# Optimization experiments

Hardware: AMD Instinct MI355X
Metric: run time of the kernel (lower is better)

The kernel has to match this reference:

```python
import jax, jax.numpy as jnp
import numpy as np

# Dimensions: T total prefill tokens, S ragged segments (one adapter each),
# M target modules sharing this linear, r LoRA rank.
T, D_IN, D_OUT, R, M, S = 8192, 4096, 4096, 16, 2, 8


def setup_inputs() -> dict:
    key = jax.random.key(0)
    ks = jax.random.split(key, 6)
    x = jax.random.normal(ks[0], (T, D_IN), dtype=jnp.float32)
    W = jax.random.normal(ks[1], (D_OUT, D_IN), dtype=jnp.float32) * 0.02
    b = jax.random.normal(ks[2], (D_OUT,), dtype=jnp.float32) * 0.02
    # lora_A[m, s] = A.T of adapter s for target module m: [D_IN, R]
    lora_A = jax.random.normal(ks[3], (M, S, D_IN, R), dtype=jnp.float32) * 0.02
    # lora_B[m, s] = B.T: [R, D_OUT]
    lora_B = jax.random.normal(ks[4], (M, S, R, D_OUT), dtype=jnp.float32) * 0.02
    cu = jnp.sort(jax.random.randint(ks[5], (S + 1,), 0, T + 1, dtype=jnp.int32))
    cu = cu.at[0].set(0).at[-1].set(T)  # segment boundaries cover [0, T)
    return {"x": x, "W": W, "b": b, "lora_A": lora_A, "lora_B": lora_B,
            "cu_seqlen": cu}


def reference(x, W, b, lora_A, lora_B, cu_seqlen):
    # Base linear: out = x @ W.T + b
    out = x @ W.T + b
    tok = jnp.arange(x.shape[0])
    n_seg = lora_A.shape[1]
    # SGMV-style ragged LoRA: tokens in segment s use adapter s for every
    # target module m; contributions from all modules add into `out`.
    # Masking (instead of dynamic slicing) keeps shapes static / jit-friendly
    # and is exact: masked-out tokens contribute zero.
    for s in range(n_seg):
        mask = ((tok >= cu_seqlen[s]) & (tok < cu_seqlen[s + 1]))
        xm = x * mask.astype(x.dtype)[:, None]            # [T, D_IN], zero outside segment
        u = jnp.einsum('td,mdr->tmr', xm, lora_A[:, s])    # [T, M, R] low-rank down-proj
        out = out + jnp.einsum('tmr,mrD->tD', u, lora_B[:, s])  # up-proj, sum over modules
    return out
```

## Files before the change

kernel.cpp:

```cpp
#include <hip/hip_runtime.h>
#include <hip/hip_bf16.h>

#define T_TOK 8192
#define DIN   4096
#define DOUT  4096
#define RANK  16
#define NMOD  2
#define NSEG  8

typedef __attribute__((ext_vector_type(8))) short bf16x8;
typedef __attribute__((ext_vector_type(8))) unsigned short u16x8;
typedef __attribute__((ext_vector_type(4))) float f32x4;

__device__ inline unsigned short f2bf(float f) {
    union { float f; unsigned u; } v; v.f = f;
    unsigned r = v.u + 0x7FFFu + ((v.u >> 16) & 1u);
    return (unsigned short)(r >> 16);
}

__device__ inline void gload_lds16(const void* g, void* l) {
    __builtin_amdgcn_global_load_lds(
        (const __attribute__((address_space(1))) void*)g,
        (__attribute__((address_space(3))) void*)l, 16, 0, 0);
}

__global__ void cast2_bf16_kernel(const float* __restrict__ sa,
                                  unsigned short* __restrict__ da, int n8a,
                                  const float* __restrict__ sb,
                                  unsigned short* __restrict__ db, int n8b) {
    int i = blockIdx.x * blockDim.x + threadIdx.x;
    const float* s;
    unsigned short* d;
    size_t j;
    if (i < n8a) { s = sa; d = da; j = (size_t)i; }
    else if (i < n8a + n8b) { s = sb; d = db; j = (size_t)(i - n8a); }
    else return;
    const float4* s4 = (const float4*)s;
    float4 a = s4[2 * j];
    float4 b = s4[2 * j + 1];
    u16x8 o;
    o[0] = f2bf(a.x); o[1] = f2bf(a.y); o[2] = f2bf(a.z); o[3] = f2bf(a.w);
    o[4] = f2bf(b.x); o[5] = f2bf(b.y); o[6] = f2bf(b.z); o[7] = f2bf(b.w);
    *(u16x8*)(d + 8 * j) = o;
}

__global__ void prep_A_kernel(const float* __restrict__ A,
                              unsigned short* __restrict__ At) {
    int idx = blockIdx.x * 256 + threadIdx.x;
    int d   = idx & (DIN - 1);
    int smr = idx >> 12;
    int s   = smr >> 5, mr = smr & 31;
    int m   = mr >> 4,  r  = mr & 15;
    float v = A[(((size_t)(m * NSEG + s) * DIN) + d) * RANK + r];
    At[idx] = f2bf(v);
}

__global__ void prep_B_kernel(const float* __restrict__ B,
                              unsigned short* __restrict__ Bt) {
    int o  = blockIdx.x * 256 + threadIdx.x;
    int s  = o >> 12;
    int oc = o & (DOUT - 1);
    unsigned short tmp[32];
    for (int m = 0; m < NMOD; ++m)
        for (int r = 0; r < RANK; ++r)
            tmp[m * 16 + r] =
                f2bf(B[(((size_t)(m * NSEG + s) * RANK) + r) * DOUT + oc]);
    for (int k = 0; k < 4; ++k) {
        u16x8 v;
        for (int j = 0; j < 8; ++j) v[j] = tmp[k * 8 + j];
        *(u16x8*)(Bt + (size_t)o * 32 + k * 8) = v;
    }
}

__global__ __launch_bounds__(64) void u_gemm_kernel(
    const unsigned short* __restrict__ xb, const unsigned short* __restrict__ At,
    const int* __restrict__ cu, float* __restrict__ Pu) {
    int tile = blockIdx.x;
    int ky   = blockIdx.y;
    int lane = threadIdx.x;
    int l15  = lane & 15, lk = lane >> 4;
    int t0   = tile * 32;
    f32x4 acc[2][2] = {};
    bf16x8 zero = {};
    for (int s = 0; s < NSEG; ++s) {
        int lo = cu[s], hi = cu[s + 1];
        if (hi <= t0 || lo >= t0 + 32) continue;
        const unsigned short* atb = At + (size_t)(s * 32) * DIN;
        for (int kt = 0; kt < 32; ++kt) {
            int k0 = ky * 1024 + kt * 32 + lk * 8;
            bf16x8 a[2], b[2];
            for (int mi = 0; mi < 2; ++mi) {
                int row = t0 + mi * 16 + l15;
                bf16x8 av = *(const bf16x8*)(xb + (size_t)row * DIN + k0);
                a[mi] = (row >= lo && row < hi) ? av : zero;
            }
            for (int ni = 0; ni < 2; ++ni) {
                int mr = ni * 16 + l15;
                b[ni] = *(const bf16x8*)(atb + (size_t)mr * DIN + k0);
            }
            for (int mi = 0; mi < 2; ++mi)
                for (int ni = 0; ni < 2; ++ni)
                    acc[mi][ni] = __builtin_amdgcn_mfma_f32_16x16x32_bf16(
                        a[mi], b[ni], acc[mi][ni], 0, 0, 0);
        }
    }
    for (int mi = 0; mi < 2; ++mi)
        for (int ni = 0; ni < 2; ++ni)
            for (int j = 0; j < 4; ++j) {
                int t  = t0 + mi * 16 + lk * 4 + j;
                int mr = ni * 16 + l15;
                Pu[((size_t)ky * T_TOK + t) * 32 + mr] = acc[mi][ni][j];
            }
}

__global__ void reduce_u_kernel(const float* __restrict__ Pu,
                                unsigned short* __restrict__ ub) {
    int idx = blockIdx.x * 256 + threadIdx.x;
    const size_t STRIDE = (size_t)T_TOK * 32;
    float s = Pu[idx] + Pu[idx + STRIDE] + Pu[idx + 2 * STRIDE] + Pu[idx + 3 * STRIDE];
    ub[idx] = f2bf(s);
}


__device__ __forceinline__ bf16x8 lds_frag(const char* tile, int row, int lk) {
    int rb = (row << 6) + (lk << 4);
    rb ^= ((rb >> 7) & 7) << 4;
    return *(const bf16x8*)(tile + rb);
}

__device__ __forceinline__ void stage_chunk(const unsigned short* gbase,
                                            char* lds_tile, int chunkbase, int tid) {
    int tb = chunkbase + tid * 16;
    int gb = tb ^ (((tb >> 7) & 7) << 4);
    int row = gb >> 6;
    int col = (gb & 63) >> 1;
    gload_lds16(gbase + (size_t)row * DIN + col, lds_tile + tb);
}

#define STAGE(T_)                                                              \
  {                                                                            \
    int k0s_ = (T_) * 32;                                                      \
    char* dst_ = lds + ((T_) & 3) * 32768;                                     \
    stage_chunk(xrow + k0s_, dst_, 0, tid);                                    \
    stage_chunk(xrow + k0s_, dst_, 8192, tid);                                 \
    stage_chunk(wrow_g + k0s_, dst_ + 16384, 0, tid);                          \
    stage_chunk(wrow_g + k0s_, dst_ + 16384, 8192, tid);                       \
  }

#define READ_AF2(T_)                                                           \
  {                                                                            \
    const char* Asl_ = lds + ((T_) & 3) * 32768;                               \
    for (int m = 0; m < 4; ++m)                                                \
        af2[m] = lds_frag(Asl_, wrow + (4 + m) * 16 + l15, lk);                \
  }

#define READ_MAIN(BFR_, AF_, T_)                                               \
  {                                                                            \
    const char* Asl_ = lds + ((T_) & 3) * 32768;                               \
    const char* Bsl_ = Asl_ + 16384;                                           \
    for (int n = 0; n < 4; ++n)                                                \
        BFR_[n] = lds_frag(Bsl_, wcol + n * 16 + l15, lk);                     \
    for (int m = 0; m < 4; ++m)                                                \
        AF_[m] = lds_frag(Asl_, wrow + m * 16 + l15, lk);                      \
  }

#define CLUSTER(BFR_, AF_)                                                     \
  {                                                                            \
    __builtin_amdgcn_s_setprio(1);                                             \
    for (int m = 0; m < 4; ++m)                                                \
        for (int n = 0; n < 4; ++n)                                            \
            acc[m][n] = __builtin_amdgcn_mfma_f32_16x16x32_bf16(               \
                AF_[m], BFR_[n], acc[m][n], 0, 0, 0);                          \
    for (int m = 0; m < 4; ++m)                                                \
        for (int n = 0; n < 4; ++n)                                            \
            acc[4 + m][n] = __builtin_amdgcn_mfma_f32_16x16x32_bf16(           \
                af2[m], BFR_[n], acc[4 + m][n], 0, 0, 0);                      \
    __builtin_amdgcn_s_setprio(0);                                             \
  }

#define ITER(UB_, UA_, RB_, RA_, T_, STG_, VM_)                                \
  {                                                                            \
    READ_AF2(T_);                                                              \
    READ_MAIN(RB_, RA_, (T_) + 1);                                             \
    if (STG_) STAGE((T_) + 3);                                                 \
    __builtin_amdgcn_sched_barrier(0);                                         \
    CLUSTER(UB_, UA_);                                                         \
    if ((VM_) == 4)      asm volatile("s_waitcnt vmcnt(4)" ::: "memory");      \
    else if ((VM_) == 0) asm volatile("s_waitcnt vmcnt(0)" ::: "memory");      \
    if ((VM_) >= 0) __builtin_amdgcn_s_barrier();                              \
  }

__global__ __launch_bounds__(512, 2) void main_gemm_kernel(
    const unsigned short* __restrict__ xb, const unsigned short* __restrict__ wb,
    const unsigned short* __restrict__ ub, const unsigned short* __restrict__ bt,
    const float* __restrict__ bias, const int* __restrict__ cu,
    float* __restrict__ out) {
    __shared__ __attribute__((aligned(1024))) char lds[131072];
    int tid  = threadIdx.x;
    int w    = tid >> 6, lane = tid & 63;
    int l15  = lane & 15, lk = lane >> 4;
    int wrow = (w >> 2) * 128;
    int wcol = (w & 3) * 64;
    int swz  = (blockIdx.x & 7) * 64 + (blockIdx.x >> 3);
    int row0 = (swz >> 4) * 256;
    int col0 = (swz & 15) * 256;

    const unsigned short* xrow   = xb + (size_t)row0 * DIN;
    const unsigned short* wrow_g = wb + (size_t)col0 * DIN;

    f32x4 acc[8][4] = {};
    bf16x8 bfrA[4], afA[4], bfrB[4], afB[4], af2[4];

    STAGE(0); STAGE(1); STAGE(2);
    asm volatile("s_waitcnt vmcnt(4)" ::: "memory");
    __builtin_amdgcn_s_barrier();
    READ_MAIN(bfrA, afA, 0);

    #pragma unroll 1
    for (int t = 0; t < 124; t += 2) {
        ITER(bfrA, afA, bfrB, afB, t,     1, 4);
        ITER(bfrB, afB, bfrA, afA, t + 1, 1, 4);
    }
    ITER(bfrA, afA, bfrB, afB, 124, 1, 4);
    ITER(bfrB, afB, bfrA, afA, 125, 0, 0);
    ITER(bfrA, afA, bfrB, afB, 126, 0, -1);
    { READ_AF2(127); __builtin_amdgcn_sched_barrier(0); CLUSTER(bfrB, afB); }

    bf16x8 zero = {};
    for (int s = 0; s < NSEG; ++s) {
        int lo = cu[s], hi = cu[s + 1];
        if (hi <= row0 || lo >= row0 + 256) continue;
        bf16x8 au[8], bu[4];
        for (int m = 0; m < 8; ++m) {
            int row = row0 + wrow + m * 16 + l15;
            bf16x8 v = *(const bf16x8*)(ub + (size_t)row * 32 + lk * 8);
            au[m] = (row >= lo && row < hi) ? v : zero;
        }
        for (int n = 0; n < 4; ++n) {
            int col = col0 + wcol + n * 16 + l15;
            bu[n] = *(const bf16x8*)(bt + ((size_t)s * DOUT + col) * 32 + lk * 8);
        }
        for (int m = 0; m < 8; ++m)
            for (int n = 0; n < 4; ++n)
                acc[m][n] = __builtin_amdgcn_mfma_f32_16x16x32_bf16(
                    au[m], bu[n], acc[m][n], 0, 0, 0);
    }

    float bv[4];
    for (int n = 0; n < 4; ++n) bv[n] = bias[col0 + wcol + n * 16 + l15];
    for (int m = 0; m < 8; ++m) {
        int rbase = row0 + wrow + m * 16 + lk * 4;
        for (int n = 0; n < 4; ++n) {
            int col = col0 + wcol + n * 16 + l15;
            for (int jj = 0; jj < 4; ++jj)
                out[(size_t)(rbase + jj) * DOUT + col] = acc[m][n][jj] + bv[n];
        }
    }
}

extern "C" void kernel_launch(void* const* d_in, const int* in_sizes, int n_in,
                              void* d_out, int out_size, void* d_ws, size_t ws_size,
                              hipStream_t stream) {
    const float* x  = (const float*)d_in[0];
    const float* W  = (const float*)d_in[1];
    const float* b  = (const float*)d_in[2];
    const float* lA = (const float*)d_in[3];
    const float* lB = (const float*)d_in[4];
    const int*   cu = (const int*)d_in[5];
    float* out = (float*)d_out;

    char* ws = (char*)d_ws;
    unsigned short* xb = (unsigned short*)(ws);
    unsigned short* wb = (unsigned short*)(ws + 67108864);
    unsigned short* At = (unsigned short*)(ws + 100663296);
    unsigned short* Bt = (unsigned short*)(ws + 102760448);
    float*          Pu = (float*)(ws + 104857600);
    unsigned short* ub = (unsigned short*)(ws + 109051904);

    const int n8x = T_TOK * DIN / 8, n8w = DOUT * DIN / 8;
    cast2_bf16_kernel<<<(n8x + n8w) / 256, 256, 0, stream>>>(x, xb, n8x, W, wb, n8w);
    prep_A_kernel<<<(NSEG * 32 * DIN) / 256, 256, 0, stream>>>(lA, At);
    prep_B_kernel<<<(NSEG * DOUT) / 256, 256, 0, stream>>>(lB, Bt);
    dim3 ug(T_TOK / 32, 4);
    u_gemm_kernel<<<ug, 64, 0, stream>>>(xb, At, cu, Pu);
    reduce_u_kernel<<<(T_TOK * 32) / 256, 256, 0, stream>>>(Pu, ub);
    dim3 mg(32 * 16);
    main_gemm_kernel<<<mg, 512, 0, stream>>>(xb, wb, ub, Bt, b, cu, out);
}
```

Measured before the change: 326.6 us.

## Switch main GEMM from 16x16x32 to 32x32x16 bf16 MFMA tiles

Replaces the 16x16x32 MFMA tiling of the per-wave 128x64 output tile with 32x32x16 instructions, restructuring the LDS fragment reads, accumulator layout, LoRA up-projection MFMAs and the epilogue store mapping. The larger MFMA shape needs fewer LDS fragment loads per FLOP and fewer instructions, aiming to raise matrix-core throughput. The cost is a different register layout for the accumulators and a more scattered epilogue write pattern, and the 32-wide instructions have longer latency to hide.

```diff
diff --git a/kernel.cpp b/kernel.cpp
--- a/kernel.cpp
+++ b/kernel.cpp
@@ -11,6 +11,7 @@
 typedef __attribute__((ext_vector_type(8))) short bf16x8;
 typedef __attribute__((ext_vector_type(8))) unsigned short u16x8;
 typedef __attribute__((ext_vector_type(4))) float f32x4;
+typedef __attribute__((ext_vector_type(16))) float f32x16;
 
 __device__ inline unsigned short f2bf(float f) {
     union { float f; unsigned u; } v; v.f = f;
@@ -122,8 +123,8 @@
 }
 
 
-__device__ __forceinline__ bf16x8 lds_frag(const char* tile, int row, int lk) {
-    int rb = (row << 6) + (lk << 4);
+__device__ __forceinline__ bf16x8 lds_frag32(const char* tile, int row, int kb) {
+    int rb = (row << 6) + kb;
     rb ^= ((rb >> 7) & 7) << 4;
     return *(const bf16x8*)(tile + rb);
 }
@@ -147,41 +148,43 @@
     stage_chunk(wrow_g + k0s_, dst_ + 16384, 8192, tid);                       \
   }
 
-#define READ_AF2(T_)                                                           \
+#define READ_AH1(T_)                                                           \
   {                                                                            \
     const char* Asl_ = lds + ((T_) & 3) * 32768;                               \
     for (int m = 0; m < 4; ++m)                                                \
-        af2[m] = lds_frag(Asl_, wrow + (4 + m) * 16 + l15, lk);                \
-  }
-
-#define READ_MAIN(BFR_, AF_, T_)                                               \
+        af2[m] = lds_frag32(Asl_, wrow + m * 32 + l31, 32 + kb16);             \
+  }
+
+#define READ_NEXT(BFR_, AF_, T_)                                               \
   {                                                                            \
     const char* Asl_ = lds + ((T_) & 3) * 32768;                               \
     const char* Bsl_ = Asl_ + 16384;                                           \
-    for (int n = 0; n < 4; ++n)                                                \
-        BFR_[n] = lds_frag(Bsl_, wcol + n * 16 + l15, lk);                     \
+    for (int n = 0; n < 2; ++n) {                                              \
+        BFR_[n][0] = lds_frag32(Bsl_, wcol + n * 32 + l31, kb16);              \
+        BFR_[n][1] = lds_frag32(Bsl_, wcol + n * 32 + l31, 32 + kb16);         \
+    }                                                                          \
     for (int m = 0; m < 4; ++m)                                                \
-        AF_[m] = lds_frag(Asl_, wrow + m * 16 + l15, lk);                      \
+        AF_[m] = lds_frag32(Asl_, wrow + m * 32 + l31, kb16);                  \
   }
 
 #define CLUSTER(BFR_, AF_)                                                     \
   {                                                                            \
     __builtin_amdgcn_s_setprio(1);                                             \
     for (int m = 0; m < 4; ++m)                                                \
-        for (int n = 0; n < 4; ++n)                                            \
-            acc[m][n] = __builtin_amdgcn_mfma_f32_16x16x32_bf16(               \
-                AF_[m], BFR_[n], acc[m][n], 0, 0, 0);                          \
+        for (int n = 0; n < 2; ++n)                                            \
+            acc[m][n] = __builtin_amdgcn_mfma_f32_32x32x16_bf16(               \
+                AF_[m], BFR_[n][0], acc[m][n], 0, 0, 0);                       \
     for (int m = 0; m < 4; ++m)                                                \
-        for (int n = 0; n < 4; ++n)                                            \
-            acc[4 + m][n] = __builtin_amdgcn_mfma_f32_16x16x32_bf16(           \
-                af2[m], BFR_[n], acc[4 + m][n], 0, 0, 0);                      \
+        for (int n = 0; n < 2; ++n)                                            \
+            acc[m][n] = __builtin_amdgcn_mfma_f32_32x32x16_bf16(               \
+                af2[m], BFR_[n][1], acc[m][n], 0, 0, 0);                       \
     __builtin_amdgcn_s_setprio(0);                                             \
   }
 
 #define ITER(UB_, UA_, RB_, RA_, T_, STG_, VM_)                                \
   {                                                                            \
-    READ_AF2(T_);                                                              \
-    READ_MAIN(RB_, RA_, (T_) + 1);                                             \
+    READ_AH1(T_);                                                              \
+    READ_NEXT(RB_, RA_, (T_) + 1);                                             \
     if (STG_) STAGE((T_) + 3);                                                 \
     __builtin_amdgcn_sched_barrier(0);                                         \
     CLUSTER(UB_, UA_);                                                         \
@@ -198,7 +201,8 @@
     __shared__ __attribute__((aligned(1024))) char lds[131072];
     int tid  = threadIdx.x;
     int w    = tid >> 6, lane = tid & 63;
-    int l15  = lane & 15, lk = lane >> 4;
+    int l31  = lane & 31;
+    int kb16 = (lane >> 5) * 16;
     int wrow = (w >> 2) * 128;
     int wcol = (w & 3) * 64;
     int swz  = (blockIdx.x & 7) * 64 + (blockIdx.x >> 3);
@@ -208,13 +212,13 @@
     const unsigned short* xrow   = xb + (size_t)row0 * DIN;
     const unsigned short* wrow_g = wb + (size_t)col0 * DIN;
 
-    f32x4 acc[8][4] = {};
-    bf16x8 bfrA[4], afA[4], bfrB[4], afB[4], af2[4];
+    f32x16 acc[4][2] = {};
+    bf16x8 bfrA[2][2], afA[4], bfrB[2][2], afB[4], af2[4];
 
     STAGE(0); STAGE(1); STAGE(2);
     asm volatile("s_waitcnt vmcnt(4)" ::: "memory");
     __builtin_amdgcn_s_barrier();
-    READ_MAIN(bfrA, afA, 0);
+    READ_NEXT(bfrA, afA, 0);
 
     #pragma unroll 1
     for (int t = 0; t < 124; t += 2) {
@@ -224,36 +228,47 @@
     ITER(bfrA, afA, bfrB, afB, 124, 1, 4);
     ITER(bfrB, afB, bfrA, afA, 125, 0, 0);
     ITER(bfrA, afA, bfrB, afB, 126, 0, -1);
-    { READ_AF2(127); __builtin_amdgcn_sched_barrier(0); CLUSTER(bfrB, afB); }
+    { READ_AH1(127); __builtin_amdgcn_sched_barrier(0); CLUSTER(bfrB, afB); }
 
     bf16x8 zero = {};
     for (int s = 0; s < NSEG; ++s) {
         int lo = cu[s], hi = cu[s + 1];
         if (hi <= row0 || lo >= row0 + 256) continue;
-        bf16x8 au[8], bu[4];
-        for (int m = 0; m < 8; ++m) {
-            int row = row0 + wrow + m * 16 + l15;
-            bf16x8 v = *(const bf16x8*)(ub + (size_t)row * 32 + lk * 8);
-            au[m] = (row >= lo && row < hi) ? v : zero;
+        bf16x8 au[4][2], bu[2][2];
+        for (int m = 0; m < 4; ++m) {
+            int row = row0 + wrow + m * 32 + l31;
+            const char* ubase = (const char*)ub + (size_t)row * 64;
+            bf16x8 v0 = *(const bf16x8*)(ubase + kb16);
+            bf16x8 v1 = *(const bf16x8*)(ubase + 32 + kb16);
+            bool in = (row >= lo && row < hi);
+            au[m][0] = in ? v0 : zero;
+            au[m][1] = in ? v1 : zero;
         }
-        for (int n = 0; n < 4; ++n) {
-            int col = col0 + wcol + n * 16 + l15;
-            bu[n] = *(const bf16x8*)(bt + ((size_t)s * DOUT + col) * 32 + lk * 8);
+        for (int n = 0; n < 2; ++n) {
+            int col = col0 + wcol + n * 32 + l31;
+            const char* bbase = (const char*)bt + ((size_t)s * DOUT + col) * 64;
+            bu[n][0] = *(const bf16x8*)(bbase + kb16);
+            bu[n][1] = *(const bf16x8*)(bbase + 32 + kb16);
         }
-        for (int m = 0; m < 8; ++m)
-            for (int n = 0; n < 4; ++n)
-                acc[m][n] = __builtin_amdgcn_mfma_f32_16x16x32_bf16(
-                    au[m], bu[n], acc[m][n], 0, 0, 0);
-    }
-
-    float bv[4];
-    for (int n = 0; n < 4; ++n) bv[n] = bias[col0 + wcol + n * 16 + l15];
-    for (int m = 0; m < 8; ++m) {
-        int rbase = row0 + wrow + m * 16 + lk * 4;
-        for (int n = 0; n < 4; ++n) {
-            int col = col0 + wcol + n * 16 + l15;
-            for (int jj = 0; jj < 4; ++jj)
-                out[(size_t)(rbase + jj) * DOUT + col] = acc[m][n][jj] + bv[n];
+        for (int h = 0; h < 2; ++h)
+            for (int m = 0; m < 4; ++m)
+                for (int n = 0; n < 2; ++n)
+                    acc[m][n] = __builtin_amdgcn_mfma_f32_32x32x16_bf16(
+                        au[m][h], bu[n][h], acc[m][n], 0, 0, 0);
+    }
+
+    float bv[2];
+    for (int n = 0; n < 2; ++n) bv[n] = bias[col0 + wcol + n * 32 + l31];
+    int rsub = 4 * (lane >> 5);
+    for (int m = 0; m < 4; ++m) {
+        int rbase = row0 + wrow + m * 32 + rsub;
+        for (int n = 0; n < 2; ++n) {
+            int col = col0 + wcol + n * 32 + l31;
+            #pragma unroll
+            for (int r = 0; r < 16; ++r) {
+                int row = rbase + (r & 3) + 8 * (r >> 2);
+                out[(size_t)row * DOUT + col] = acc[m][n][r] + bv[n];
+            }
         }
     }
 }
```

Result: slower. 353.5 us (+8.2%).

## Restructure main GEMM into 64-wide K double-buffer with four-phase ping-pong schedule

Applied to the files above, without the earlier changes.

The main bf16 GEMM loop moves from a 4-deep ring of 32-wide K tiles to a 2-deep double buffer of 64-wide K tiles. Each K step is split into four MFMA phases, each with a barrier and a priority bump. Global-to-LDS staging for the next tile is interleaved across those phases, and the LDS swizzle uses 128-byte rows. The aim is fewer loop iterations and better overlap of loads with MFMA work, at the cost of more barriers per step and a shallower prefetch depth.

```diff
diff --git a/kernel.cpp b/kernel.cpp
--- a/kernel.cpp
+++ b/kernel.cpp
@@ -122,72 +122,87 @@
 }
 
 
-__device__ __forceinline__ bf16x8 lds_frag(const char* tile, int row, int lk) {
-    int rb = (row << 6) + (lk << 4);
+__device__ __forceinline__ bf16x8 frag(const char* mat, int row, int kbyte) {
+    int rb = (row << 7) + kbyte;
     rb ^= ((rb >> 7) & 7) << 4;
-    return *(const bf16x8*)(tile + rb);
-}
-
-__device__ __forceinline__ void stage_chunk(const unsigned short* gbase,
-                                            char* lds_tile, int chunkbase, int tid) {
-    int tb = chunkbase + tid * 16;
-    int gb = tb ^ (((tb >> 7) & 7) << 4);
-    int row = gb >> 6;
-    int col = (gb & 63) >> 1;
-    gload_lds16(gbase + (size_t)row * DIN + col, lds_tile + tb);
-}
-
-#define STAGE(T_)                                                              \
+    return *(const bf16x8*)(mat + rb);
+}
+
+#define STAGE_B(SB_, C_, K0_)                                                  \
+  { int tb = tid * 16;                                                         \
+    int lrow = (C_)*64 + (tb >> 7);                                            \
+    int cb = (tb & 127) ^ ((lrow & 7) << 4);                                   \
+    gload_lds16(wrow_g + (size_t)lrow * DIN + (K0_) + (cb >> 1),               \
+                (SB_) + (C_)*8192 + tb); }
+
+#define STAGE_A(SA_, C_, GB_, K0_)                                             \
+  { int tb = tid * 16;                                                         \
+    int lrow = (C_)*64 + (tb >> 7);                                            \
+    int cb = (tb & 127) ^ ((lrow & 7) << 4);                                   \
+    gload_lds16(xrow + (size_t)((GB_) + (tb >> 7)) * DIN + (K0_) + (cb >> 1),  \
+                (SA_) + (C_)*8192 + tb); }
+
+#define VMC(N_)                                                                \
+    if ((N_) == 2)      asm volatile("s_waitcnt vmcnt(2)" ::: "memory");       \
+    else if ((N_) == 0) asm volatile("s_waitcnt vmcnt(0)" ::: "memory");
+
+#define PH_TAIL(VM_)                                                           \
+    __builtin_amdgcn_s_barrier();                                              \
+    asm volatile("s_waitcnt lgkmcnt(0)" ::: "memory");                         \
+    __builtin_amdgcn_sched_barrier(0);                                         \
+    __builtin_amdgcn_s_setprio(1);
+
+#define PH_END(VM_)                                                            \
+    __builtin_amdgcn_s_setprio(0);                                             \
+    VMC(VM_);                                                                  \
+    __builtin_amdgcn_s_barrier();
+
+#define KSTEP(T_, CB_, STG_, VM0_, VM3_)                                       \
   {                                                                            \
-    int k0s_ = (T_) * 32;                                                      \
-    char* dst_ = lds + ((T_) & 3) * 32768;                                     \
-    stage_chunk(xrow + k0s_, dst_, 0, tid);                                    \
-    stage_chunk(xrow + k0s_, dst_, 8192, tid);                                 \
-    stage_chunk(wrow_g + k0s_, dst_ + 16384, 0, tid);                          \
-    stage_chunk(wrow_g + k0s_, dst_ + 16384, 8192, tid);                       \
-  }
-
-#define READ_AF2(T_)                                                           \
-  {                                                                            \
-    const char* Asl_ = lds + ((T_) & 3) * 32768;                               \
+    const char* cA  = lds + (CB_)*65536;                                       \
+    const char* cBm = cA + 32768;                                              \
+    char* sA = lds + (1 - (CB_))*65536;                                        \
+    char* sB = sA + 32768;                                                     \
+    const int k0n = ((T_) + 1) * 64;                                           \
+    bf16x8 af[4], bf0[4], bf1[4];                                              \
+    \
+    for (int n = 0; n < 4; ++n) bf0[n] = frag(cBm, wcol + n*16 + l15, lk*16);  \
+    for (int m = 0; m < 4; ++m) af[m]  = frag(cA, whalf*64 + m*16 + l15, lk*16);\
+    if (STG_) { STAGE_B(sB, 0, k0n); STAGE_B(sB, 1, k0n); }                    \
+    PH_TAIL(VM0_);                                                             \
+    for (int m = 0; m < 4; ++m) for (int n = 0; n < 4; ++n)                    \
+        acc[m][n] = __builtin_amdgcn_mfma_f32_16x16x32_bf16(                   \
+            af[m], bf0[n], acc[m][n], 0, 0, 0);                                \
+    PH_END(VM0_);                                                              \
+           \
     for (int m = 0; m < 4; ++m)                                                \
-        af2[m] = lds_frag(Asl_, wrow + (4 + m) * 16 + l15, lk);                \
-  }
-
-#define READ_MAIN(BFR_, AF_, T_)                                               \
-  {                                                                            \
-    const char* Asl_ = lds + ((T_) & 3) * 32768;                               \
-    const char* Bsl_ = Asl_ + 16384;                                           \
+        af[m] = frag(cA, 128 + whalf*64 + m*16 + l15, lk*16);                  \
+    if (STG_) { STAGE_B(sB, 2, k0n); STAGE_B(sB, 3, k0n); }                    \
+    PH_TAIL(-1);                                                               \
+    for (int m = 0; m < 4; ++m) for (int n = 0; n < 4; ++n)                    \
+        acc[4 + m][n] = __builtin_amdgcn_mfma_f32_16x16x32_bf16(               \
+            af[m], bf0[n], acc[4 + m][n], 0, 0, 0);                            \
+    PH_END(-1);                                                                \
+    \
     for (int n = 0; n < 4; ++n)                                                \
-        BFR_[n] = lds_frag(Bsl_, wcol + n * 16 + l15, lk);                     \
+        bf1[n] = frag(cBm, wcol + n*16 + l15, 64 + lk*16);                     \
     for (int m = 0; m < 4; ++m)                                                \
-        AF_[m] = lds_frag(Asl_, wrow + m * 16 + l15, lk);                      \
-  }
-
-#define CLUSTER(BFR_, AF_)                                                     \
-  {                                                                            \
-    __builtin_amdgcn_s_setprio(1);                                             \
+        af[m] = frag(cA, whalf*64 + m*16 + l15, 64 + lk*16);                   \
+    if (STG_) { STAGE_A(sA, 0, 0, k0n); STAGE_A(sA, 1, 128, k0n); }            \
+    PH_TAIL(-1);                                                               \
+    for (int m = 0; m < 4; ++m) for (int n = 0; n < 4; ++n)                    \
+        acc[m][n] = __builtin_amdgcn_mfma_f32_16x16x32_bf16(                   \
+            af[m], bf1[n], acc[m][n], 0, 0, 0);                                \
+    PH_END(-1);                                                                \
+           \
     for (int m = 0; m < 4; ++m)                                                \
-        for (int n = 0; n < 4; ++n)                                            \
-            acc[m][n] = __builtin_amdgcn_mfma_f32_16x16x32_bf16(               \
-                AF_[m], BFR_[n], acc[m][n], 0, 0, 0);                          \
-    for (int m = 0; m < 4; ++m)                                                \
-        for (int n = 0; n < 4; ++n)                                            \
-            acc[4 + m][n] = __builtin_amdgcn_mfma_f32_16x16x32_bf16(           \
-                af2[m], BFR_[n], acc[4 + m][n], 0, 0, 0);                      \
-    __builtin_amdgcn_s_setprio(0);                                             \
-  }
-
-#define ITER(UB_, UA_, RB_, RA_, T_, STG_, VM_)                                \
-  {                                                                            \
-    READ_AF2(T_);                                                              \
-    READ_MAIN(RB_, RA_, (T_) + 1);                                             \
-    if (STG_) STAGE((T_) + 3);                                                 \
-    __builtin_amdgcn_sched_barrier(0);                                         \
-    CLUSTER(UB_, UA_);                                                         \
-    if ((VM_) == 4)      asm volatile("s_waitcnt vmcnt(4)" ::: "memory");      \
-    else if ((VM_) == 0) asm volatile("s_waitcnt vmcnt(0)" ::: "memory");      \
-    if ((VM_) >= 0) __builtin_amdgcn_s_barrier();                              \
+        af[m] = frag(cA, 128 + whalf*64 + m*16 + l15, 64 + lk*16);             \
+    if (STG_) { STAGE_A(sA, 2, 64, k0n); STAGE_A(sA, 3, 192, k0n); }           \
+    PH_TAIL(VM3_);                                                             \
+    for (int m = 0; m < 4; ++m) for (int n = 0; n < 4; ++n)                    \
+        acc[4 + m][n] = __builtin_amdgcn_mfma_f32_16x16x32_bf16(               \
+            af[m], bf1[n], acc[4 + m][n], 0, 0, 0);                            \
+    PH_END(VM3_);                                                              \
   }
 
 __global__ __launch_bounds__(512, 2) void main_gemm_kernel(
@@ -196,11 +211,12 @@
     const float* __restrict__ bias, const int* __restrict__ cu,
     float* __restrict__ out) {
     __shared__ __attribute__((aligned(1024))) char lds[131072];
-    int tid  = threadIdx.x;
-    int w    = tid >> 6, lane = tid & 63;
-    int l15  = lane & 15, lk = lane >> 4;
-    int wrow = (w >> 2) * 128;
-    int wcol = (w & 3) * 64;
+    int tid   = threadIdx.x;
+    int w     = tid >> 6, lane = tid & 63;
+    int l15   = lane & 15, lk = lane >> 4;
+    int whalf = w >> 2;
+    int wrow  = whalf * 128;
+    int wcol  = (w & 3) * 64;
     int swz  = (blockIdx.x & 7) * 64 + (blockIdx.x >> 3);
     int row0 = (swz >> 4) * 256;
     int col0 = (swz & 15) * 256;
@@ -209,22 +225,25 @@
     const unsigned short* wrow_g = wb + (size_t)col0 * DIN;
 
     f32x4 acc[8][4] = {};
-    bf16x8 bfrA[4], afA[4], bfrB[4], afB[4], af2[4];
-
-    STAGE(0); STAGE(1); STAGE(2);
-    asm volatile("s_waitcnt vmcnt(4)" ::: "memory");
+
+    {
+        char* sA = lds;
+        char* sB = lds + 32768;
+        STAGE_B(sB, 0, 0); STAGE_B(sB, 1, 0);
+        STAGE_B(sB, 2, 0); STAGE_B(sB, 3, 0);
+        STAGE_A(sA, 0, 0, 0); STAGE_A(sA, 1, 128, 0);
+        STAGE_A(sA, 2, 64, 0); STAGE_A(sA, 3, 192, 0);
+    }
+    asm volatile("s_waitcnt vmcnt(2)" ::: "memory");
     __builtin_amdgcn_s_barrier();
-    READ_MAIN(bfrA, afA, 0);
 
     #pragma unroll 1
-    for (int t = 0; t < 124; t += 2) {
-        ITER(bfrA, afA, bfrB, afB, t,     1, 4);
-        ITER(bfrB, afB, bfrA, afA, t + 1, 1, 4);
-    }
-    ITER(bfrA, afA, bfrB, afB, 124, 1, 4);
-    ITER(bfrB, afB, bfrA, afA, 125, 0, 0);
-    ITER(bfrA, afA, bfrB, afB, 126, 0, -1);
-    { READ_AF2(127); __builtin_amdgcn_sched_barrier(0); CLUSTER(bfrB, afB); }
+    for (int t = 0; t < 62; t += 2) {
+        KSTEP(t,     0, 1, 2, 2);
+        KSTEP(t + 1, 1, 1, 2, 2);
+    }
+    KSTEP(62, 0, 1, 2, 2);
+    KSTEP(63, 1, 0, 0, -1);
 
     bf16x8 zero = {};
     for (int s = 0; s < NSEG; ++s) {
```

New measurement: 316.0 us. 3.3% less time.

## Pre-tile W into MFMA fragment layout and load B fragments directly from global

Applied to the files above, without the earlier changes.

The W cast kernel now writes bf16 W in a fragment-tiled layout, so each lane's B operand is one contiguous 16-byte global load. The main GEMM no longer stages W through LDS. Only x tiles go through a 4-slot LDS ring, which halves LDS use, and the pipeline is reordered around the direct B register loads. The block-to-tile mapping is changed so that blocks on each XCD share weight column panels, which should improve L2 reuse. The risk is that direct global B loads are exposed to latency and are not shared between waves in a block, which raises L2 traffic.

```diff
diff --git a/kernel.cpp b/kernel.cpp
--- a/kernel.cpp
+++ b/kernel.cpp
@@ -29,19 +29,27 @@
                                   const float* __restrict__ sb,
                                   unsigned short* __restrict__ db, int n8b) {
     int i = blockIdx.x * blockDim.x + threadIdx.x;
-    const float* s;
-    unsigned short* d;
-    size_t j;
-    if (i < n8a) { s = sa; d = da; j = (size_t)i; }
-    else if (i < n8a + n8b) { s = sb; d = db; j = (size_t)(i - n8a); }
-    else return;
-    const float4* s4 = (const float4*)s;
-    float4 a = s4[2 * j];
-    float4 b = s4[2 * j + 1];
-    u16x8 o;
-    o[0] = f2bf(a.x); o[1] = f2bf(a.y); o[2] = f2bf(a.z); o[3] = f2bf(a.w);
-    o[4] = f2bf(b.x); o[5] = f2bf(b.y); o[6] = f2bf(b.z); o[7] = f2bf(b.w);
-    *(u16x8*)(d + 8 * j) = o;
+    if (i < n8a) {
+        size_t j = (size_t)i;
+        const float4* s4 = (const float4*)sa;
+        float4 a = s4[2 * j], b = s4[2 * j + 1];
+        u16x8 o;
+        o[0] = f2bf(a.x); o[1] = f2bf(a.y); o[2] = f2bf(a.z); o[3] = f2bf(a.w);
+        o[4] = f2bf(b.x); o[5] = f2bf(b.y); o[6] = f2bf(b.z); o[7] = f2bf(b.w);
+        *(u16x8*)(da + 8 * j) = o;
+    } else if (i < n8a + n8b) {
+        size_t j = (size_t)(i - n8a);
+        const float4* s4 = (const float4*)sb;
+        float4 a = s4[2 * j], b = s4[2 * j + 1];
+        u16x8 o;
+        o[0] = f2bf(a.x); o[1] = f2bf(a.y); o[2] = f2bf(a.z); o[3] = f2bf(a.w);
+        o[4] = f2bf(b.x); o[5] = f2bf(b.y); o[6] = f2bf(b.z); o[7] = f2bf(b.w);
+        int row = (int)(j >> 9);
+        int kc  = ((int)j & 511) << 3;
+        int ct = row >> 4, c = row & 15, kt = kc >> 5, lk = (kc >> 3) & 3;
+        size_t dst = ((size_t)(ct * 128 + kt) << 9) + c * 32 + lk * 8;
+        *(u16x8*)(db + dst) = o;
+    }
 }
 
 __global__ void prep_A_kernel(const float* __restrict__ A,
@@ -122,109 +130,92 @@
 }
 
 
-__device__ __forceinline__ bf16x8 lds_frag(const char* tile, int row, int lk) {
-    int rb = (row << 6) + (lk << 4);
-    rb ^= ((rb >> 7) & 7) << 4;
-    return *(const bf16x8*)(tile + rb);
-}
-
-__device__ __forceinline__ void stage_chunk(const unsigned short* gbase,
-                                            char* lds_tile, int chunkbase, int tid) {
-    int tb = chunkbase + tid * 16;
-    int gb = tb ^ (((tb >> 7) & 7) << 4);
-    int row = gb >> 6;
-    int col = (gb & 63) >> 1;
-    gload_lds16(gbase + (size_t)row * DIN + col, lds_tile + tb);
-}
-
-#define STAGE(T_)                                                              \
+__device__ __forceinline__ bf16x8 fragA(const char* slot, int row, int lk) {
+    int rb = (row << 6) + ((lk ^ ((row >> 1) & 3)) << 4);
+    return *(const bf16x8*)(slot + rb);
+}
+
+#define STAGE_A(T_)                                                            \
+  { char* dst_ = ldsA + ((T_) & 3) * 16384;                                    \
+    int k0_ = (T_) * 32;                                                       \
+    { int tb = tid * 16;                                                       \
+      int lrow = tb >> 6;                                                      \
+      int cb = (tb & 63) ^ ((((lrow) >> 1) & 3) << 4);                         \
+      gload_lds16(xrow + (size_t)lrow * DIN + k0_ + (cb >> 1), dst_ + tb); }   \
+    { int tb = 8192 + tid * 16;                                                \
+      int lrow = tb >> 6;                                                      \
+      int cb = (tb & 63) ^ ((((lrow) >> 1) & 3) << 4);                         \
+      gload_lds16(xrow + (size_t)lrow * DIN + k0_ + (cb >> 1), dst_ + tb); } }
+
+#define BLOAD(BR_, KT_)                                                        \
+    for (int n = 0; n < 4; ++n)                                                \
+        BR_[n] = *(const bf16x8*)(wbt +                                        \
+            (((size_t)(ctb + n) * 128 + (KT_)) << 9) + l15 * 32 + lk * 8);
+
+#define LDSREAD(AR_, T_)                                                       \
+  { const char* slot_ = ldsA + ((T_) & 3) * 16384;                             \
+    for (int m = 0; m < 8; ++m)                                                \
+        AR_[m] = fragA(slot_, wrow + m * 16 + l15, lk); }
+
+#define VMW(N_)                                                                \
+    if ((N_) == 6)      asm volatile("s_waitcnt vmcnt(6)" ::: "memory");       \
+    else if ((N_) == 4) asm volatile("s_waitcnt vmcnt(4)" ::: "memory");       \
+    else if ((N_) == 0) asm volatile("s_waitcnt vmcnt(0)" ::: "memory");
+
+#define ITER(AU_, BU_, AR_, BR_, T_, STG_, RD_, VM_, BAR_)                     \
   {                                                                            \
-    int k0s_ = (T_) * 32;                                                      \
-    char* dst_ = lds + ((T_) & 3) * 32768;                                     \
-    stage_chunk(xrow + k0s_, dst_, 0, tid);                                    \
-    stage_chunk(xrow + k0s_, dst_, 8192, tid);                                 \
-    stage_chunk(wrow_g + k0s_, dst_ + 16384, 0, tid);                          \
-    stage_chunk(wrow_g + k0s_, dst_ + 16384, 8192, tid);                       \
-  }
-
-#define READ_AF2(T_)                                                           \
-  {                                                                            \
-    const char* Asl_ = lds + ((T_) & 3) * 32768;                               \
-    for (int m = 0; m < 4; ++m)                                                \
-        af2[m] = lds_frag(Asl_, wrow + (4 + m) * 16 + l15, lk);                \
-  }
-
-#define READ_MAIN(BFR_, AF_, T_)                                               \
-  {                                                                            \
-    const char* Asl_ = lds + ((T_) & 3) * 32768;                               \
-    const char* Bsl_ = Asl_ + 16384;                                           \
-    for (int n = 0; n < 4; ++n)                                                \
-        BFR_[n] = lds_frag(Bsl_, wcol + n * 16 + l15, lk);                     \
-    for (int m = 0; m < 4; ++m)                                                \
-        AF_[m] = lds_frag(Asl_, wrow + m * 16 + l15, lk);                      \
-  }
-
-#define CLUSTER(BFR_, AF_)                                                     \
-  {                                                                            \
+    if (STG_) STAGE_A((T_) + 3);                                               \
+    __builtin_amdgcn_sched_barrier(0);                                         \
+    if (RD_) { BLOAD(BR_, (T_) + 1); LDSREAD(AR_, (T_) + 1); }                 \
+    __builtin_amdgcn_sched_barrier(0);                                         \
+    VMW(VM_);                                                                  \
     __builtin_amdgcn_s_setprio(1);                                             \
-    for (int m = 0; m < 4; ++m)                                                \
+    for (int m = 0; m < 8; ++m)                                                \
         for (int n = 0; n < 4; ++n)                                            \
             acc[m][n] = __builtin_amdgcn_mfma_f32_16x16x32_bf16(               \
-                AF_[m], BFR_[n], acc[m][n], 0, 0, 0);                          \
-    for (int m = 0; m < 4; ++m)                                                \
-        for (int n = 0; n < 4; ++n)                                            \
-            acc[4 + m][n] = __builtin_amdgcn_mfma_f32_16x16x32_bf16(           \
-                af2[m], BFR_[n], acc[4 + m][n], 0, 0, 0);                      \
+                AU_[m], BU_[n], acc[m][n], 0, 0, 0);                           \
     __builtin_amdgcn_s_setprio(0);                                             \
+    if (BAR_) __builtin_amdgcn_s_barrier();                                    \
   }
 
-#define ITER(UB_, UA_, RB_, RA_, T_, STG_, VM_)                                \
-  {                                                                            \
-    READ_AF2(T_);                                                              \
-    READ_MAIN(RB_, RA_, (T_) + 1);                                             \
-    if (STG_) STAGE((T_) + 3);                                                 \
-    __builtin_amdgcn_sched_barrier(0);                                         \
-    CLUSTER(UB_, UA_);                                                         \
-    if ((VM_) == 4)      asm volatile("s_waitcnt vmcnt(4)" ::: "memory");      \
-    else if ((VM_) == 0) asm volatile("s_waitcnt vmcnt(0)" ::: "memory");      \
-    if ((VM_) >= 0) __builtin_amdgcn_s_barrier();                              \
-  }
-
 __global__ __launch_bounds__(512, 2) void main_gemm_kernel(
-    const unsigned short* __restrict__ xb, const unsigned short* __restrict__ wb,
+    const unsigned short* __restrict__ xb, const unsigned short* __restrict__ wbt,
     const unsigned short* __restrict__ ub, const unsigned short* __restrict__ bt,
     const float* __restrict__ bias, const int* __restrict__ cu,
     float* __restrict__ out) {
-    __shared__ __attribute__((aligned(1024))) char lds[131072];
+    __shared__ __attribute__((aligned(1024))) char ldsA[65536];
     int tid  = threadIdx.x;
     int w    = tid >> 6, lane = tid & 63;
     int l15  = lane & 15, lk = lane >> 4;
     int wrow = (w >> 2) * 128;
     int wcol = (w & 3) * 64;
-    int swz  = (blockIdx.x & 7) * 64 + (blockIdx.x >> 3);
-    int row0 = (swz >> 4) * 256;
-    int col0 = (swz & 15) * 256;
-
-    const unsigned short* xrow   = xb + (size_t)row0 * DIN;
-    const unsigned short* wrow_g = wb + (size_t)col0 * DIN;
+    int xcd  = blockIdx.x & 7, local = blockIdx.x >> 3;
+    int colp = xcd + 8 * (local >> 5);
+    int rowp = local & 31;
+    int row0 = rowp * 256, col0 = colp * 256;
+    int ctb  = colp * 16 + (w & 3) * 4;
+
+    const unsigned short* xrow = xb + (size_t)row0 * DIN;
 
     f32x4 acc[8][4] = {};
-    bf16x8 bfrA[4], afA[4], bfrB[4], afB[4], af2[4];
-
-    STAGE(0); STAGE(1); STAGE(2);
-    asm volatile("s_waitcnt vmcnt(4)" ::: "memory");
+    bf16x8 afA[8], afB[8], bfA[4], bfB[4];
+
+    STAGE_A(0); STAGE_A(1); STAGE_A(2);
+    __builtin_amdgcn_sched_barrier(0);
+    BLOAD(bfA, 0);
+    asm volatile("s_waitcnt vmcnt(0)" ::: "memory");
     __builtin_amdgcn_s_barrier();
-    READ_MAIN(bfrA, afA, 0);
+    LDSREAD(afA, 0);
 
     #pragma unroll 1
     for (int t = 0; t < 124; t += 2) {
-        ITER(bfrA, afA, bfrB, afB, t,     1, 4);
-        ITER(bfrB, afB, bfrA, afA, t + 1, 1, 4);
-    }
-    ITER(bfrA, afA, bfrB, afB, 124, 1, 4);
-    ITER(bfrB, afB, bfrA, afA, 125, 0, 0);
-    ITER(bfrA, afA, bfrB, afB, 126, 0, -1);
-    { READ_AF2(127); __builtin_amdgcn_sched_barrier(0); CLUSTER(bfrB, afB); }
+        ITER(afA, bfA, afB, bfB, t,     1, 1, 6, 1);
+        ITER(afB, bfB, afA, bfA, t + 1, 1, 1, 6, 1);
+    }
+    ITER(afA, bfA, afB, bfB, 124, 1, 1, 6, 1);
+    ITER(afB, bfB, afA, bfA, 125, 0, 1, 4, 1);
+    ITER(afA, bfA, afB, bfB, 126, 0, 1, 4, 1);
+    ITER(afB, bfB, afA, bfA, 127, 0, 0, 0, 0);
 
     bf16x8 zero = {};
     for (int s = 0; s < NSEG; ++s) {
@@ -270,20 +261,20 @@
     float* out = (float*)d_out;
 
     char* ws = (char*)d_ws;
-    unsigned short* xb = (unsigned short*)(ws);
-    unsigned short* wb = (unsigned short*)(ws + 67108864);
-    unsigned short* At = (unsigned short*)(ws + 100663296);
-    unsigned short* Bt = (unsigned short*)(ws + 102760448);
-    float*          Pu = (float*)(ws + 104857600);
-    unsigned short* ub = (unsigned short*)(ws + 109051904);
+    unsigned short* xb  = (unsigned short*)(ws);
+    unsigned short* wbt = (unsigned short*)(ws + 67108864);
+    unsigned short* At  = (unsigned short*)(ws + 100663296);
+    unsigned short* Bt  = (unsigned short*)(ws + 102760448);
+    float*          Pu  = (float*)(ws + 104857600);
+    unsigned short* ub  = (unsigned short*)(ws + 109051904);
 
     const int n8x = T_TOK * DIN / 8, n8w = DOUT * DIN / 8;
-    cast2_bf16_kernel<<<(n8x + n8w) / 256, 256, 0, stream>>>(x, xb, n8x, W, wb, n8w);
+    cast2_bf16_kernel<<<(n8x + n8w) / 256, 256, 0, stream>>>(x, xb, n8x, W, wbt, n8w);
     prep_A_kernel<<<(NSEG * 32 * DIN) / 256, 256, 0, stream>>>(lA, At);
     prep_B_kernel<<<(NSEG * DOUT) / 256, 256, 0, stream>>>(lB, Bt);
     dim3 ug(T_TOK / 32, 4);
     u_gemm_kernel<<<ug, 64, 0, stream>>>(xb, At, cu, Pu);
     reduce_u_kernel<<<(T_TOK * 32) / 256, 256, 0, stream>>>(Pu, ub);
     dim3 mg(32 * 16);
-    main_gemm_kernel<<<mg, 512, 0, stream>>>(xb, wb, ub, Bt, b, cu, out);
-}
+    main_gemm_kernel<<<mg, 512, 0, stream>>>(xb, wbt, ub, Bt, b, cu, out);
+}
```

Result: slower. 389.1 us (+19.1%).
